# Kernel tuning notes

Hardware: AMD Instinct MI355X
Metric: run time of the kernel (lower is better)

## Reference

```python
import jax, jax.numpy as jnp
import numpy as np

N_ACTORS = 50000
N_EDGES = 800000
D = 128
L = 2
EDGE_IN = 2 * D + 2  # src feat + rel (x,y) + dst feat


def setup_inputs() -> dict:
    key = jax.random.key(0)
    ks = jax.random.split(key, 6)
    actor_features = jax.random.normal(ks[0], (N_ACTORS, D), dtype=jnp.float32)
    edge_dist_rel = jax.random.normal(ks[1], (N_EDGES, 2), dtype=jnp.float32)
    # per-layer learned weights (bias=False in both Linears)
    W_att = jax.random.normal(ks[2], (L, EDGE_IN), dtype=jnp.float32) * 0.05
    W_emb = jax.random.normal(ks[3], (L, D, EDGE_IN), dtype=jnp.float32) * 0.05
    edge_src_idx = jax.random.randint(ks[4], (N_EDGES,), 0, N_ACTORS, dtype=jnp.int32)
    edge_dst_idx = jax.random.randint(ks[5], (N_EDGES,), 0, N_ACTORS, dtype=jnp.int32)
    return {
        "actor_features": actor_features,
        "edge_dist_rel": edge_dist_rel,
        "W_att": W_att,
        "W_emb": W_emb,
        "edge_src_idx": edge_src_idx,
        "edge_dst_idx": edge_dst_idx,
    }


def _scatter_softmax(scores, dst_idx, num_segments):
    # numerically stable softmax over irregular dst groups
    seg_max = jax.ops.segment_max(scores, dst_idx, num_segments=num_segments)
    ex = jnp.exp(scores - seg_max[dst_idx])
    denom = jax.ops.segment_sum(ex, dst_idx, num_segments=num_segments)
    return ex / denom[dst_idx]


def reference(actor_features, edge_dist_rel, W_att, W_emb, edge_src_idx, edge_dst_idx):
    n = actor_features.shape[0]
    feat = actor_features
    for l in range(W_att.shape[0]):  # small fixed number of layers
        # gather per-edge features and build edge inputs [E, 2D+2]
        e_in = jnp.concatenate(
            [feat[edge_src_idx], edge_dist_rel, feat[edge_dst_idx]], axis=-1)
        # edge attention: Linear(edge_in -> 1, no bias) + LeakyReLU(0.2)
        s = jax.nn.leaky_relu(e_in @ W_att[l], negative_slope=0.2)  # [E]
        att = _scatter_softmax(s, edge_dst_idx, n)  # dropout omitted (eval mode)
        # edge embed: Linear(edge_in -> D, no bias)
        emb = e_in @ W_emb[l].T  # [E, D]
        agg = jax.ops.segment_sum(att[:, None] * emb, edge_dst_idx, num_segments=n)
        feat = jax.nn.relu(agg)
    return feat
```

## Files before the change

### kernel.cpp

```cpp
#include <hip/hip_runtime.h>
#include <hip/hip_fp16.h>

#define D 128
#define EDGE_IN 258
#define TI 32

__device__ __forceinline__ float rl_f(float v, int j) {
  return __int_as_float(__builtin_amdgcn_readlane(__float_as_int(v), j));
}
__device__ __forceinline__ int rl_i(int v, int j) {
  return __builtin_amdgcn_readlane(v, j);
}

__global__ void zero_int(int* __restrict__ p, int n) {
  int i = blockIdx.x * blockDim.x + threadIdx.x;
  if (i < n) p[i] = 0;
}

__global__ void hist_kernel(const int* __restrict__ dst, int* __restrict__ deg, int ne) {
  int e = blockIdx.x * blockDim.x + threadIdx.x;
  if (e < ne) atomicAdd(&deg[dst[e]], 1);
}

__global__ __launch_bounds__(256) void scan_part(const int* __restrict__ deg,
                                                 int* __restrict__ bsum, int n) {
  __shared__ int red[256];
  int b = blockIdx.x, tid = threadIdx.x;
  int base = b * 1024 + tid * 4;
  int s = 0;
#pragma unroll
  for (int j = 0; j < 4; j++) { int idx = base + j; if (idx < n) s += deg[idx]; }
  red[tid] = s;
  __syncthreads();
  for (int off = 128; off; off >>= 1) {
    if (tid < off) red[tid] += red[tid + off];
    __syncthreads();
  }
  if (tid == 0) bsum[b] = red[0];
}

__global__ __launch_bounds__(256) void scan_bsums(int* __restrict__ bsum, int nb) {
  __shared__ int part[256];
  int tid = threadIdx.x;
  int v = (tid < nb) ? bsum[tid] : 0;
  part[tid] = v;
  __syncthreads();
  for (int off = 1; off < 256; off <<= 1) {
    int t = (tid >= off) ? part[tid - off] : 0;
    __syncthreads();
    part[tid] += t;
    __syncthreads();
  }
  if (tid < nb) bsum[tid] = (tid == 0) ? 0 : part[tid - 1];
}

__global__ __launch_bounds__(256) void scan_final(const int* __restrict__ deg,
                                                  const int* __restrict__ bsumex,
                                                  int* __restrict__ offs,
                                                  int* __restrict__ cur, int n, int ne) {
  __shared__ int part[256];
  int b = blockIdx.x, tid = threadIdx.x;
  int base = b * 1024 + tid * 4;
  int v[4];
  int s = 0;
#pragma unroll
  for (int j = 0; j < 4; j++) {
    int idx = base + j;
    v[j] = (idx < n) ? deg[idx] : 0;
    s += v[j];
  }
  part[tid] = s;
  __syncthreads();
  for (int off = 1; off < 256; off <<= 1) {
    int t = (tid >= off) ? part[tid - off] : 0;
    __syncthreads();
    part[tid] += t;
    __syncthreads();
  }
  int run = bsumex[b] + ((tid == 0) ? 0 : part[tid - 1]);
#pragma unroll
  for (int j = 0; j < 4; j++) {
    int idx = base + j;
    if (idx < n) { offs[idx] = run; cur[idx] = run; run += v[j]; }
  }
  if (b == 0 && tid == 0) offs[n] = ne;
}

__global__ void scatter_kernel(const int* __restrict__ dst, const int* __restrict__ srcIdx,
                               const float2* __restrict__ rel, int* __restrict__ cur,
                               float4* __restrict__ meta, int ne) {
  int e = blockIdx.x * blockDim.x + threadIdx.x;
  if (e < ne) {
    int p = atomicAdd(&cur[dst[e]], 1);
    float2 r = rel[e];
    meta[p] = make_float4(__int_as_float(srcIdx[e]), r.x, r.y, 0.f);
  }
}

__global__ void transpose_kernel(const float* __restrict__ W_emb, float* __restrict__ WT,
                                 float* __restrict__ Wrel) {
  int d = threadIdx.x;
  int k = blockIdx.x;
  int part = blockIdx.y;
  int l = blockIdx.z;
  if (part < 2) {
    int off = part ? 130 : 0;
    int mat = l * 2 + part;
    WT[((mat * 32 + (k >> 2)) * 128 + d) * 4 + (k & 3)] =
        W_emb[(size_t)(l * D + d) * EDGE_IN + off + k];
  } else if (k < 2) {
    Wrel[(l * 2 + k) * 128 + d] = W_emb[(size_t)(l * D + d) * EDGE_IN + 128 + k];
  }
}

__global__ __launch_bounds__(256) void proj_kernel(const float* __restrict__ feat,
                                                   const float4* __restrict__ WT,
                                                   __half* __restrict__ Ps16,
                                                   float* __restrict__ Pd, int n, int l) {
  __shared__ float lf[TI][D];
  int i0 = blockIdx.x * TI;
  int tid = threadIdx.x;
  for (int t = tid; t < TI * D / 4; t += 256) {
    int fi = t >> 5;
    int gi = i0 + fi;
    float4 v = (gi < n) ? ((const float4*)feat)[(size_t)gi * (D / 4) + (t & 31)]
                        : make_float4(0.f, 0.f, 0.f, 0.f);
    ((float4*)&lf[0][0])[t] = v;
  }
  __syncthreads();
  int d = tid & (D - 1);
  int g = tid >> 7;
  const float4* WsT4 = WT + (size_t)(l * 2 + 0) * 32 * 128;
  const float4* WdT4 = WT + (size_t)(l * 2 + 1) * 32 * 128;
  float accs[16], accd[16];
#pragma unroll
  for (int i = 0; i < 16; i++) { accs[i] = 0.f; accd[i] = 0.f; }
  int ibase = g * 16;
  for (int k4 = 0; k4 < 32; k4++) {
    float4 ws = WsT4[k4 * 128 + d];
    float4 wd = WdT4[k4 * 128 + d];
#pragma unroll
    for (int i = 0; i < 16; i++) {
      float4 f = *(const float4*)&lf[ibase + i][k4 * 4];
      accs[i] += f.x * ws.x + f.y * ws.y + f.z * ws.z + f.w * ws.w;
      accd[i] += f.x * wd.x + f.y * wd.y + f.z * wd.z + f.w * wd.w;
    }
  }
#pragma unroll
  for (int i = 0; i < 16; i++) {
    int gi = i0 + ibase + i;
    if (gi < n) {
      Ps16[(size_t)gi * D + d] = __float2half(accs[i]);
      Pd[(size_t)gi * D + d] = accd[i];
    }
  }
}

__global__ __launch_bounds__(256) void att_proj(const float* __restrict__ feat,
                                                const float* __restrict__ W_att,
                                                float* __restrict__ a_s,
                                                float* __restrict__ a_d, int n, int l) {
  int i = blockIdx.x * blockDim.x + threadIdx.x;
  if (i >= n) return;
  const float* Wa = W_att + (size_t)l * EDGE_IN;
  const float4* f = (const float4*)(feat + (size_t)i * D);
  float s = 0.f, t = 0.f;
#pragma unroll 8
  for (int k4 = 0; k4 < 32; k4++) {
    float4 v = f[k4];
    int k = 4 * k4;
    s += v.x * Wa[k] + v.y * Wa[k + 1] + v.z * Wa[k + 2] + v.w * Wa[k + 3];
    t += v.x * Wa[130 + k] + v.y * Wa[131 + k] + v.z * Wa[132 + k] + v.w * Wa[133 + k];
  }
  a_s[i] = s;
  a_d[i] = t;
}

__global__ __launch_bounds__(256) void edge_kernel(
    const __half2* __restrict__ Ps, const float* __restrict__ Pd,
    const float* __restrict__ a_s, const float* __restrict__ a_d,
    const float4* __restrict__ meta, const int* __restrict__ offs,
    const float* __restrict__ Wrel, const float* __restrict__ W_att,
    float* __restrict__ out, int n, int l) {
  int wid = (blockIdx.x * blockDim.x + threadIdx.x) >> 6;
  if (wid >= n) return;
  int lane = threadIdx.x & 63;
  int d0 = 2 * lane;
  const float2 wc0 = *(const float2*)&Wrel[(l * 2 + 0) * 128 + d0];
  const float2 wc1 = *(const float2*)&Wrel[(l * 2 + 1) * 128 + d0];
  float wax = W_att[(size_t)l * EDGE_IN + 128];
  float way = W_att[(size_t)l * EDGE_IN + 129];
  float ad = a_d[wid];
  int p0 = offs[wid], p1 = offs[wid + 1];
  float m = -1e30f, lsum = 0.f;
  float accx = 0.f, accy = 0.f;
  for (int c0 = p0; c0 < p1; c0 += 64) {
    int cn = min(64, p1 - c0);
    int si = 0;
    float rx = 0.f, ry = 0.f, s = -1e30f;
    if (lane < cn) {
      float4 mt = meta[c0 + lane];
      si = __float_as_int(mt.x);
      rx = mt.y;
      ry = mt.z;
      float sc = a_s[si] + ad + rx * wax + ry * way;
      s = (sc > 0.f) ? sc : 0.2f * sc;
    }
    float cm = s;
#pragma unroll
    for (int o = 32; o; o >>= 1) cm = fmaxf(cm, __shfl_xor(cm, o, 64));
    float mnew = fmaxf(m, cm);
    float corrOld = __expf(m - mnew);
    float w = (lane < cn) ? __expf(s - mnew) : 0.f;
    float csum = w;
#pragma unroll
    for (int o = 32; o; o >>= 1) csum += __shfl_xor(csum, o, 64);
    lsum = lsum * corrOld + csum;
    accx *= corrOld;
    accy *= corrOld;
    m = mnew;
    int j = 0;
    for (; j + 4 <= cn; j += 4) {
      int s0 = rl_i(si, j), s1 = rl_i(si, j + 1), s2 = rl_i(si, j + 2), s3 = rl_i(si, j + 3);
      float w0 = rl_f(w, j), w1 = rl_f(w, j + 1), w2 = rl_f(w, j + 2), w3 = rl_f(w, j + 3);
      float x0 = rl_f(rx, j), x1 = rl_f(rx, j + 1), x2 = rl_f(rx, j + 2), x3 = rl_f(rx, j + 3);
      float y0 = rl_f(ry, j), y1 = rl_f(ry, j + 1), y2 = rl_f(ry, j + 2), y3 = rl_f(ry, j + 3);
      __half2 h0 = Ps[(size_t)s0 * 64 + lane];
      __half2 h1 = Ps[(size_t)s1 * 64 + lane];
      __half2 h2 = Ps[(size_t)s2 * 64 + lane];
      __half2 h3 = Ps[(size_t)s3 * 64 + lane];
      float2 f0 = __half22float2(h0), f1 = __half22float2(h1);
      float2 f2 = __half22float2(h2), f3 = __half22float2(h3);
      accx += w0 * (f0.x + x0 * wc0.x + y0 * wc1.x);
      accy += w0 * (f0.y + x0 * wc0.y + y0 * wc1.y);
      accx += w1 * (f1.x + x1 * wc0.x + y1 * wc1.x);
      accy += w1 * (f1.y + x1 * wc0.y + y1 * wc1.y);
      accx += w2 * (f2.x + x2 * wc0.x + y2 * wc1.x);
      accy += w2 * (f2.y + x2 * wc0.y + y2 * wc1.y);
      accx += w3 * (f3.x + x3 * wc0.x + y3 * wc1.x);
      accy += w3 * (f3.y + x3 * wc0.y + y3 * wc1.y);
    }
    for (; j < cn; j++) {
      int sj = rl_i(si, j);
      float wj = rl_f(w, j), xj = rl_f(rx, j), yj = rl_f(ry, j);
      float2 fj = __half22float2(Ps[(size_t)sj * 64 + lane]);
      accx += wj * (fj.x + xj * wc0.x + yj * wc1.x);
      accy += wj * (fj.y + xj * wc0.y + yj * wc1.y);
    }
  }
  float2 o2 = make_float2(0.f, 0.f);
  if (p1 > p0) {
    float inv = 1.0f / lsum;
    float2 pd = *(const float2*)&Pd[(size_t)wid * D + d0];
    o2.x = fmaxf(accx * inv + pd.x, 0.f);
    o2.y = fmaxf(accy * inv + pd.y, 0.f);
  }
  *(float2*)&out[(size_t)wid * D + d0] = o2;
}

extern "C" void kernel_launch(void* const* d_in, const int* in_sizes, int n_in,
                              void* d_out, int out_size, void* d_ws, size_t ws_size,
                              hipStream_t stream) {
  const float* actor = (const float*)d_in[0];
  const float* rel   = (const float*)d_in[1];
  const float* W_att = (const float*)d_in[2];
  const float* W_emb = (const float*)d_in[3];
  const int* srcIdx  = (const int*)d_in[4];
  const int* dstIdx  = (const int*)d_in[5];
  int n  = in_sizes[0] / D;
  int ne = in_sizes[4];
  int Lnum = in_sizes[2] / EDGE_IN;
  float* fout_last = (float*)d_out;

  float* ws = (float*)d_ws;
  size_t o = 0;
  float4* meta = (float4*)ws; o += 4 * (size_t)ne;
  float* WT  = ws + o; o += (size_t)Lnum * 2 * 128 * 128;
  float* Wre = ws + o; o += (size_t)Lnum * 2 * 128;
  float* Pd  = ws + o; o += (size_t)n * D;
  float* a_s = ws + o; o += (size_t)n + 64;
  float* a_d = ws + o; o += (size_t)n + 64;
  __half* Ps16 = (__half*)(ws + o); o += (size_t)n * D / 2;
  int* ibuf = (int*)(ws + o);
  size_t io = 0;
  int* deg  = ibuf + io; io += n + 64;
  int* offs = ibuf + io; io += n + 64;
  int* cur  = ibuf + io; io += n + 64;
  int* bsum = ibuf + io; io += 256;

  int nb = (n + 1023) / 1024;

  zero_int<<<(n + 255) / 256, 256, 0, stream>>>(deg, n);
  hist_kernel<<<(ne + 255) / 256, 256, 0, stream>>>(dstIdx, deg, ne);
  scan_part<<<nb, 256, 0, stream>>>(deg, bsum, n);
  scan_bsums<<<1, 256, 0, stream>>>(bsum, nb);
  scan_final<<<nb, 256, 0, stream>>>(deg, bsum, offs, cur, n, ne);
  scatter_kernel<<<(ne + 255) / 256, 256, 0, stream>>>(dstIdx, srcIdx, (const float2*)rel,
                                                       cur, meta, ne);
  transpose_kernel<<<dim3(128, 3, Lnum), 128, 0, stream>>>(W_emb, WT, Wre);

  const float* fin = actor;
  for (int l = 0; l < Lnum; l++) {
    proj_kernel<<<(n + TI - 1) / TI, 256, 0, stream>>>(fin, (const float4*)WT, Ps16, Pd, n, l);
    att_proj<<<(n + 255) / 256, 256, 0, stream>>>(fin, W_att, a_s, a_d, n, l);
    edge_kernel<<<(n + 3) / 4, 256, 0, stream>>>((const __half2*)Ps16, Pd, a_s, a_d, meta,
                                                 offs, Wre, W_att, fout_last, n, l);
    fin = fout_last;
  }
}
```

Measured before the change: 396.2 us.

## Fuse attention projection into register-tiled proj kernel, deepen edge gather unroll

Removes the separate att_proj kernel by computing the per-node attention dot products inside proj_kernel from the shared-memory feature tile, with a cross-lane reduction. proj_kernel is restructured into a 4x4 register tile per thread (4 actors x 4 output dims) with vectorized fp16 and fp32 stores. The edge kernel gather loop is unrolled to 8 so more independent loads are in flight, and the scalar tail loop becomes a predicated block. The cost is more registers per thread and a reduction step per block.

Measured after the change: 507.0 us. 1.28x slower.

```diff
diff --git a/kernel.cpp b/kernel.cpp
--- a/kernel.cpp
+++ b/kernel.cpp
@@ -10,6 +10,9 @@
 }
 __device__ __forceinline__ int rl_i(int v, int j) {
   return __builtin_amdgcn_readlane(v, j);
+}
+__device__ __forceinline__ float dot4(float4 a, float4 b) {
+  return a.x * b.x + a.y * b.y + a.z * b.z + a.w * b.w;
 }
 
 __global__ void zero_int(int* __restrict__ p, int n) {
@@ -97,8 +100,10 @@
   }
 }
 
-__global__ void transpose_kernel(const float* __restrict__ W_emb, float* __restrict__ WT,
-                                 float* __restrict__ Wrel) {
+__global__ void transpose_kernel(const float* __restrict__ W_emb,
+                                 const float* __restrict__ W_att,
+                                 float* __restrict__ WT, float* __restrict__ Wrel,
+                                 float* __restrict__ WattA) {
   int d = threadIdx.x;
   int k = blockIdx.x;
   int part = blockIdx.y;
@@ -108,15 +113,21 @@
     int mat = l * 2 + part;
     WT[((mat * 32 + (k >> 2)) * 128 + d) * 4 + (k & 3)] =
         W_emb[(size_t)(l * D + d) * EDGE_IN + off + k];
-  } else if (k < 2) {
-    Wrel[(l * 2 + k) * 128 + d] = W_emb[(size_t)(l * D + d) * EDGE_IN + 128 + k];
+  } else if (part == 2) {
+    if (k < 2) Wrel[(l * 2 + k) * 128 + d] = W_emb[(size_t)(l * D + d) * EDGE_IN + 128 + k];
+  } else if (k == 0) {
+    int off = (part == 3) ? 0 : 130;
+    WattA[(l * 2 + (part - 3)) * 128 + d] = W_att[(size_t)l * EDGE_IN + off + d];
   }
 }
 
 __global__ __launch_bounds__(256) void proj_kernel(const float* __restrict__ feat,
                                                    const float4* __restrict__ WT,
+                                                   const float* __restrict__ WattA,
                                                    __half* __restrict__ Ps16,
-                                                   float* __restrict__ Pd, int n, int l) {
+                                                   float* __restrict__ Pd,
+                                                   float* __restrict__ a_s,
+                                                   float* __restrict__ a_d, int n, int l) {
   __shared__ float lf[TI][D];
   int i0 = blockIdx.x * TI;
   int tid = threadIdx.x;
@@ -128,52 +139,69 @@
     ((float4*)&lf[0][0])[t] = v;
   }
   __syncthreads();
-  int d = tid & (D - 1);
-  int g = tid >> 7;
-  const float4* WsT4 = WT + (size_t)(l * 2 + 0) * 32 * 128;
-  const float4* WdT4 = WT + (size_t)(l * 2 + 1) * 32 * 128;
-  float accs[16], accd[16];
-#pragma unroll
-  for (int i = 0; i < 16; i++) { accs[i] = 0.f; accd[i] = 0.f; }
-  int ibase = g * 16;
+  int dg = tid & 31;
+  int ag = tid >> 5;
+  const float4* Ws = WT + (size_t)(l * 2 + 0) * 32 * 128;
+  const float4* Wd = WT + (size_t)(l * 2 + 1) * 32 * 128;
+  float accs[4][4], accd[4][4];
+#pragma unroll
+  for (int a = 0; a < 4; a++)
+#pragma unroll
+    for (int dd = 0; dd < 4; dd++) { accs[a][dd] = 0.f; accd[a][dd] = 0.f; }
+
   for (int k4 = 0; k4 < 32; k4++) {
-    float4 ws = WsT4[k4 * 128 + d];
-    float4 wd = WdT4[k4 * 128 + d];
-#pragma unroll
-    for (int i = 0; i < 16; i++) {
-      float4 f = *(const float4*)&lf[ibase + i][k4 * 4];
-      accs[i] += f.x * ws.x + f.y * ws.y + f.z * ws.z + f.w * ws.w;
-      accd[i] += f.x * wd.x + f.y * wd.y + f.z * wd.z + f.w * wd.w;
-    }
-  }
-#pragma unroll
-  for (int i = 0; i < 16; i++) {
-    int gi = i0 + ibase + i;
+    float4 fa[4], wsv[4], wdv[4];
+#pragma unroll
+    for (int a = 0; a < 4; a++) fa[a] = *(const float4*)&lf[4 * ag + a][k4 * 4];
+#pragma unroll
+    for (int dd = 0; dd < 4; dd++) {
+      wsv[dd] = Ws[k4 * 128 + 4 * dg + dd];
+      wdv[dd] = Wd[k4 * 128 + 4 * dg + dd];
+    }
+#pragma unroll
+    for (int a = 0; a < 4; a++)
+#pragma unroll
+      for (int dd = 0; dd < 4; dd++) {
+        accs[a][dd] += dot4(fa[a], wsv[dd]);
+        accd[a][dd] += dot4(fa[a], wdv[dd]);
+      }
+  }
+
+  float sa[4], ta[4];
+  {
+    float4 was = *(const float4*)&WattA[(size_t)(l * 2 + 0) * 128 + 4 * dg];
+    float4 wat = *(const float4*)&WattA[(size_t)(l * 2 + 1) * 128 + 4 * dg];
+#pragma unroll
+    for (int a = 0; a < 4; a++) {
+      float4 f = *(const float4*)&lf[4 * ag + a][4 * dg];
+      sa[a] = dot4(f, was);
+      ta[a] = dot4(f, wat);
+    }
+#pragma unroll
+    for (int o = 1; o < 32; o <<= 1) {
+#pragma unroll
+      for (int a = 0; a < 4; a++) {
+        sa[a] += __shfl_xor(sa[a], o, 64);
+        ta[a] += __shfl_xor(ta[a], o, 64);
+      }
+    }
+  }
+
+#pragma unroll
+  for (int a = 0; a < 4; a++) {
+    int gi = i0 + 4 * ag + a;
     if (gi < n) {
-      Ps16[(size_t)gi * D + d] = __float2half(accs[i]);
-      Pd[(size_t)gi * D + d] = accd[i];
-    }
-  }
-}
-
-__global__ __launch_bounds__(256) void att_proj(const float* __restrict__ feat,
-                                                const float* __restrict__ W_att,
-                                                float* __restrict__ a_s,
-                                                float* __restrict__ a_d, int n, int l) {
-  int i = blockIdx.x * blockDim.x + threadIdx.x;
-  if (i >= n) return;
-  const float* Wa = W_att + (size_t)l * EDGE_IN;
-  const float4* f = (const float4*)(feat + (size_t)i * D);
-  float s = 0.f, t = 0.f;
-#pragma unroll 8
-  for (int k4 = 0; k4 < 32; k4++) {
-    float4 v = f[k4];
-    int k = 4 * k4;
-    s += v.x * Wa[k] + v.y * Wa[k + 1] + v.z * Wa[k + 2] + v.w * Wa[k + 3];
-    t += v.x * Wa[130 + k] + v.y * Wa[131 + k] + v.z * Wa[132 + k] + v.w * Wa[133 + k];
-  }
-  a_s[i] = s;
-  a_d[i] = t;
+      ushort4 u;
+      u.x = __half_as_ushort(__float2half(accs[a][0]));
+      u.y = __half_as_ushort(__float2half(accs[a][1]));
+      u.z = __half_as_ushort(__float2half(accs[a][2]));
+      u.w = __half_as_ushort(__float2half(accs[a][3]));
+      *(ushort4*)&Ps16[(size_t)gi * D + 4 * dg] = u;
+      *(float4*)&Pd[(size_t)gi * D + 4 * dg] =
+          make_float4(accd[a][0], accd[a][1], accd[a][2], accd[a][3]);
+      if (dg == 0) { a_s[gi] = sa[a]; a_d[gi] = ta[a]; }
+    }
+  }
 }
 
 __global__ __launch_bounds__(256) void edge_kernel(
@@ -220,32 +248,44 @@
     accy *= corrOld;
     m = mnew;
     int j = 0;
-    for (; j + 4 <= cn; j += 4) {
-      int s0 = rl_i(si, j), s1 = rl_i(si, j + 1), s2 = rl_i(si, j + 2), s3 = rl_i(si, j + 3);
-      float w0 = rl_f(w, j), w1 = rl_f(w, j + 1), w2 = rl_f(w, j + 2), w3 = rl_f(w, j + 3);
-      float x0 = rl_f(rx, j), x1 = rl_f(rx, j + 1), x2 = rl_f(rx, j + 2), x3 = rl_f(rx, j + 3);
-      float y0 = rl_f(ry, j), y1 = rl_f(ry, j + 1), y2 = rl_f(ry, j + 2), y3 = rl_f(ry, j + 3);
-      __half2 h0 = Ps[(size_t)s0 * 64 + lane];
-      __half2 h1 = Ps[(size_t)s1 * 64 + lane];
-      __half2 h2 = Ps[(size_t)s2 * 64 + lane];
-      __half2 h3 = Ps[(size_t)s3 * 64 + lane];
-      float2 f0 = __half22float2(h0), f1 = __half22float2(h1);
-      float2 f2 = __half22float2(h2), f3 = __half22float2(h3);
-      accx += w0 * (f0.x + x0 * wc0.x + y0 * wc1.x);
-      accy += w0 * (f0.y + x0 * wc0.y + y0 * wc1.y);
-      accx += w1 * (f1.x + x1 * wc0.x + y1 * wc1.x);
-      accy += w1 * (f1.y + x1 * wc0.y + y1 * wc1.y);
-      accx += w2 * (f2.x + x2 * wc0.x + y2 * wc1.x);
-      accy += w2 * (f2.y + x2 * wc0.y + y2 * wc1.y);
-      accx += w3 * (f3.x + x3 * wc0.x + y3 * wc1.x);
-      accy += w3 * (f3.y + x3 * wc0.y + y3 * wc1.y);
-    }
-    for (; j < cn; j++) {
-      int sj = rl_i(si, j);
-      float wj = rl_f(w, j), xj = rl_f(rx, j), yj = rl_f(ry, j);
-      float2 fj = __half22float2(Ps[(size_t)sj * 64 + lane]);
-      accx += wj * (fj.x + xj * wc0.x + yj * wc1.x);
-      accy += wj * (fj.y + xj * wc0.y + yj * wc1.y);
+    for (; j + 8 <= cn; j += 8) {
+      float2 f[8];
+      float wj[8], xj[8], yj[8];
+#pragma unroll
+      for (int q = 0; q < 8; q++) {
+        int sj = rl_i(si, j + q);
+        wj[q] = rl_f(w, j + q);
+        xj[q] = rl_f(rx, j + q);
+        yj[q] = rl_f(ry, j + q);
+        f[q] = __half22float2(Ps[(size_t)sj * 64 + lane]);
+      }
+#pragma unroll
+      for (int q = 0; q < 8; q++) {
+        accx += wj[q] * (f[q].x + xj[q] * wc0.x + yj[q] * wc1.x);
+        accy += wj[q] * (f[q].y + xj[q] * wc0.y + yj[q] * wc1.y);
+      }
+    }
+    if (j < cn) {
+      float2 f[8];
+      float wj[8], xj[8], yj[8];
+      int r = cn - j;
+#pragma unroll
+      for (int q = 0; q < 8; q++) {
+        if (q < r) {
+          int sj = rl_i(si, j + q);
+          wj[q] = rl_f(w, j + q);
+          xj[q] = rl_f(rx, j + q);
+          yj[q] = rl_f(ry, j + q);
+          f[q] = __half22float2(Ps[(size_t)sj * 64 + lane]);
+        }
+      }
+#pragma unroll
+      for (int q = 0; q < 8; q++) {
+        if (q < r) {
+          accx += wj[q] * (f[q].x + xj[q] * wc0.x + yj[q] * wc1.x);
+          accy += wj[q] * (f[q].y + xj[q] * wc0.y + yj[q] * wc1.y);
+        }
+      }
     }
   }
   float2 o2 = make_float2(0.f, 0.f);
@@ -277,6 +317,7 @@
   float4* meta = (float4*)ws; o += 4 * (size_t)ne;
   float* WT  = ws + o; o += (size_t)Lnum * 2 * 128 * 128;
   float* Wre = ws + o; o += (size_t)Lnum * 2 * 128;
+  float* WattA = ws + o; o += (size_t)Lnum * 2 * 128;
   float* Pd  = ws + o; o += (size_t)n * D;
   float* a_s = ws + o; o += (size_t)n + 64;
   float* a_d = ws + o; o += (size_t)n + 64;
@@ -297,12 +338,12 @@
   scan_final<<<nb, 256, 0, stream>>>(deg, bsum, offs, cur, n, ne);
   scatter_kernel<<<(ne + 255) / 256, 256, 0, stream>>>(dstIdx, srcIdx, (const float2*)rel,
                                                        cur, meta, ne);
-  transpose_kernel<<<dim3(128, 3, Lnum), 128, 0, stream>>>(W_emb, WT, Wre);
+  transpose_kernel<<<dim3(128, 5, Lnum), 128, 0, stream>>>(W_emb, W_att, WT, Wre, WattA);
 
   const float* fin = actor;
   for (int l = 0; l < Lnum; l++) {
-    proj_kernel<<<(n + TI - 1) / TI, 256, 0, stream>>>(fin, (const float4*)WT, Ps16, Pd, n, l);
-    att_proj<<<(n + 255) / 256, 256, 0, stream>>>(fin, W_att, a_s, a_d, n, l);
+    proj_kernel<<<(n + TI - 1) / TI, 256, 0, stream>>>(fin, (const float4*)WT, WattA,
+                                                       Ps16, Pd, a_s, a_d, n, l);
     edge_kernel<<<(n + 3) / 4, 256, 0, stream>>>((const __half2*)Ps16, Pd, a_s, a_d, meta,
                                                  offs, Wre, W_att, fout_last, n, l);
     fin = fout_last;
```
